# Optimization experiments

Hardware: AMD Instinct MI355X
Metric: run time of the kernel (lower is better)

## Reference

```python
import jax, jax.numpy as jnp
import numpy as np

B, T_DEC, T_SRC, D = 32, 1024, 2048, 1024


def setup_inputs() -> dict:
    key = jax.random.key(0)
    k1, k2, k3 = jax.random.split(key, 3)
    decoder_outputs = jax.random.normal(k1, (B, T_DEC, D), dtype=jnp.float32)
    encoder_outputs = jax.random.normal(k2, (B, T_SRC, D), dtype=jnp.float32)
    # realistic padding mask: each batch element has a valid length in [T_SRC//2, T_SRC]
    lengths = jax.random.randint(k3, (B, 1, 1), T_SRC // 2, T_SRC + 1)
    src_mask = jnp.arange(T_SRC)[None, None, :] < lengths  # [B,1,T_SRC] bool
    return {"decoder_outputs": decoder_outputs, "encoder_outputs": encoder_outputs, "src_mask": src_mask}


def reference(decoder_outputs, encoder_outputs, src_mask):
    # scores: [B, T_dec, T_src]
    scores = jnp.einsum('btd,bsd->bts', decoder_outputs, encoder_outputs)
    scores = jnp.where(src_mask, scores, -jnp.inf)  # src_mask [B,1,T_src] broadcasts over T_dec
    attn_weights = jax.nn.softmax(scores, axis=-1)
    context = jnp.einsum('bts,bsd->btd', attn_weights, encoder_outputs)
    return context, attn_weights
```

## Files before the change

### kernel.cpp

```cpp
#include <hip/hip_runtime.h>
#include <stdint.h>

#define NB 32
#define TDEC 1024
#define TSRC 2048
#define DDIM 1024

typedef short bf16x8 __attribute__((ext_vector_type(8)));
typedef float f32x4 __attribute__((ext_vector_type(4)));


__device__ __forceinline__ unsigned short f2bf(float f) {
  union { float f; uint32_t u; } c; c.f = f;
  return (unsigned short)((c.u + 0x7FFFu + ((c.u >> 16) & 1u)) >> 16);
}

__device__ __forceinline__ void splitt(float f, unsigned short& h, unsigned short& l) {
  union { float f; uint32_t u; } c; c.f = f;
  uint32_t hb = c.u & 0xFFFF0000u;
  h = (unsigned short)(hb >> 16);
  union { uint32_t u; float f; } hf; hf.u = hb;
  union { float f; uint32_t u; } d; d.f = f - hf.f;
  l = (unsigned short)(d.u >> 16);
}

__device__ __forceinline__ int sw4(int r, int c4) {
  return (r << 6) + ((((c4 >> 3) ^ (r & 7)) << 3) | (c4 & 7));
}
__device__ __forceinline__ int sw8(int r, int c8) {
  return (r << 6) + (((c8 >> 3) ^ (r & 7)) << 3);
}

__global__ void lens_kernel(const unsigned char* __restrict__ mask,
                            int* __restrict__ lens) {
  int b = blockIdx.x;
  int tid = threadIdx.x;
  unsigned char b1 = mask[1], b3 = mask[3];
  int cnt = 0;
  if (b1 != 0) {
    const unsigned char* row = mask + (size_t)b * TSRC;
    for (int s = tid; s < TSRC; s += 256) cnt += (row[s] != 0) ? 1 : 0;
  } else if (b3 != 0) {
    const float* row = (const float*)mask + (size_t)b * TSRC;
    for (int s = tid; s < TSRC; s += 256) cnt += (row[s] != 0.0f) ? 1 : 0;
  } else {
    const int* row = (const int*)mask + (size_t)b * TSRC;
    for (int s = tid; s < TSRC; s += 256) cnt += (row[s] != 0) ? 1 : 0;
  }
#pragma unroll
  for (int o = 32; o > 0; o >>= 1) cnt += __shfl_down(cnt, o, 64);
  __shared__ int red[4];
  if ((tid & 63) == 0) red[tid >> 6] = cnt;
  __syncthreads();
  if (tid == 0) lens[b] = red[0] + red[1] + red[2] + red[3];
}

__global__ void split_kernel(const float* __restrict__ src,
                             unsigned short* __restrict__ hi,
                             unsigned short* __restrict__ lo, int n4) {
  int i = blockIdx.x * 256 + threadIdx.x;
  if (i >= n4) return;
  float4 v = *(const float4*)(src + (size_t)i * 4);
  ushort4 h, l;
  splitt(v.x, h.x, l.x); splitt(v.y, h.y, l.y);
  splitt(v.z, h.z, l.z); splitt(v.w, h.w, l.w);
  *(ushort4*)(hi + (size_t)i * 4) = h;
  *(ushort4*)(lo + (size_t)i * 4) = l;
}

__global__ void transpose_kernel(const float* __restrict__ enc,
                                 unsigned short* __restrict__ encT) {
  __shared__ float tile[64][65];
  int b = blockIdx.z;
  int s0 = blockIdx.x << 6;
  int d0 = blockIdx.y << 6;
  int tid = threadIdx.x;
  int rl = tid >> 4;
  int c4 = (tid & 15) << 2;
  const float* src = enc + ((size_t)b * TSRC + s0) * DDIM + d0;
#pragma unroll
  for (int p = 0; p < 4; ++p) {
    int s = rl + (p << 4);
    float4 v = *(const float4*)(src + (size_t)s * DDIM + c4);
    tile[s][c4 + 0] = v.x; tile[s][c4 + 1] = v.y;
    tile[s][c4 + 2] = v.z; tile[s][c4 + 3] = v.w;
  }
  __syncthreads();
  unsigned short* dst = encT + ((size_t)b * DDIM + d0) * TSRC + s0;
#pragma unroll
  for (int p = 0; p < 4; ++p) {
    int d = rl + (p << 4);
    ushort4 o;
    o.x = f2bf(tile[c4 + 0][d]);
    o.y = f2bf(tile[c4 + 1][d]);
    o.z = f2bf(tile[c4 + 2][d]);
    o.w = f2bf(tile[c4 + 3][d]);
    *(ushort4*)(dst + (size_t)d * TSRC + c4) = o;
  }
}

__global__ __launch_bounds__(256, 2) void scores_pre(
    const unsigned short* __restrict__ dhi, const unsigned short* __restrict__ dlo,
    const unsigned short* __restrict__ ehi, const unsigned short* __restrict__ elo,
    float* __restrict__ attn, const int* __restrict__ lens) {
  int b = blockIdx.z;
  int s0 = blockIdx.x << 7;
  int t0 = blockIdx.y << 7;
  if (s0 >= lens[b]) return;
  __shared__ unsigned short Ah[8192], Al[8192], Bh[8192], Bl[8192];
  const unsigned short* Ag0 = dhi + ((size_t)b * TDEC + t0) * DDIM;
  const unsigned short* Ag1 = dlo + ((size_t)b * TDEC + t0) * DDIM;
  const unsigned short* Bg0 = ehi + ((size_t)b * TSRC + s0) * DDIM;
  const unsigned short* Bg1 = elo + ((size_t)b * TSRC + s0) * DDIM;
  int tid = threadIdx.x;
  int lane = tid & 63, wid = tid >> 6;
  int wm = (wid >> 1) << 6, wn = (wid & 1) << 6;
  int fr = lane & 15, fq = lane >> 4;
  int cc8 = (tid & 7) << 3;

  f32x4 acc[16];
#pragma unroll
  for (int i = 0; i < 16; ++i) { acc[i][0] = 0.f; acc[i][1] = 0.f; acc[i][2] = 0.f; acc[i][3] = 0.f; }

  for (int kc = 0; kc < 16; ++kc) {
    int k0 = kc << 6;
    __syncthreads();
#pragma unroll
    for (int p = 0; p < 4; ++p) {
      int r = (p << 5) + (tid >> 3);
      size_t go = (size_t)r * DDIM + k0 + cc8;
      int sw = sw8(r, cc8);
      *(bf16x8*)&Ah[sw] = *(const bf16x8*)(Ag0 + go);
      *(bf16x8*)&Al[sw] = *(const bf16x8*)(Ag1 + go);
      *(bf16x8*)&Bh[sw] = *(const bf16x8*)(Bg0 + go);
      *(bf16x8*)&Bl[sw] = *(const bf16x8*)(Bg1 + go);
    }
    __syncthreads();
#pragma unroll
    for (int ks = 0; ks < 2; ++ks) {
      bf16x8 ah[4], al[4], bh[4], bl[4];
#pragma unroll
      for (int i = 0; i < 4; ++i) {
        int ra = wm + (i << 4) + fr;
        int oa = (ra << 6) + ((((ks << 2) | fq) ^ (ra & 7)) << 3);
        ah[i] = *(const bf16x8*)&Ah[oa];
        al[i] = *(const bf16x8*)&Al[oa];
        int rb = wn + (i << 4) + fr;
        int ob = (rb << 6) + ((((ks << 2) | fq) ^ (rb & 7)) << 3);
        bh[i] = *(const bf16x8*)&Bh[ob];
        bl[i] = *(const bf16x8*)&Bl[ob];
      }
#pragma unroll
      for (int mt = 0; mt < 4; ++mt)
#pragma unroll
        for (int nt = 0; nt < 4; ++nt) {
          f32x4 c = acc[(mt << 2) + nt];
          c = __builtin_amdgcn_mfma_f32_16x16x32_bf16(ah[mt], bh[nt], c, 0, 0, 0);
          c = __builtin_amdgcn_mfma_f32_16x16x32_bf16(al[mt], bh[nt], c, 0, 0, 0);
          c = __builtin_amdgcn_mfma_f32_16x16x32_bf16(ah[mt], bl[nt], c, 0, 0, 0);
          acc[(mt << 2) + nt] = c;
        }
    }
  }
  float* C = attn + ((size_t)b * TDEC + t0) * TSRC + s0;
#pragma unroll
  for (int mt = 0; mt < 4; ++mt) {
    int r0 = wm + (mt << 4) + (fq << 2);
#pragma unroll
    for (int nt = 0; nt < 4; ++nt) {
      int c0 = wn + (nt << 4) + fr;
      f32x4 v = acc[(mt << 2) + nt];
#pragma unroll
      for (int j = 0; j < 4; ++j)
        C[(size_t)(r0 + j) * TSRC + c0] = v[j];
    }
  }
}

__global__ __launch_bounds__(256, 2) void scores_fly(
    const float* __restrict__ dec, const float* __restrict__ enc,
    float* __restrict__ attn, const int* __restrict__ lens) {
  int b = blockIdx.z;
  int s0 = blockIdx.x << 7;
  int t0 = blockIdx.y << 7;
  if (s0 >= lens[b]) return;
  __shared__ unsigned short Ah[8192], Al[8192], Bh[8192], Bl[8192];
  const float* Ag = dec + ((size_t)b * TDEC + t0) * DDIM;
  const float* Bg = enc + ((size_t)b * TSRC + s0) * DDIM;
  int tid = threadIdx.x;
  int lane = tid & 63, wid = tid >> 6;
  int wm = (wid >> 1) << 6, wn = (wid & 1) << 6;
  int fr = lane & 15, fq = lane >> 4;

  f32x4 acc[16];
#pragma unroll
  for (int i = 0; i < 16; ++i) { acc[i][0] = 0.f; acc[i][1] = 0.f; acc[i][2] = 0.f; acc[i][3] = 0.f; }

  for (int kc = 0; kc < 16; ++kc) {
    int k0 = kc << 6;
    __syncthreads();
#pragma unroll
    for (int p = 0; p < 8; ++p) {
      int r = (p << 4) + (tid >> 4);
      int c4 = (tid & 15) << 2;
      size_t go = (size_t)r * DDIM + k0 + c4;
      float4 va = *(const float4*)(Ag + go);
      float4 vb = *(const float4*)(Bg + go);
      ushort4 h, l;
      splitt(va.x, h.x, l.x); splitt(va.y, h.y, l.y);
      splitt(va.z, h.z, l.z); splitt(va.w, h.w, l.w);
      int sw = sw4(r, c4);
      *(ushort4*)&Ah[sw] = h; *(ushort4*)&Al[sw] = l;
      splitt(vb.x, h.x, l.x); splitt(vb.y, h.y, l.y);
      splitt(vb.z, h.z, l.z); splitt(vb.w, h.w, l.w);
      *(ushort4*)&Bh[sw] = h; *(ushort4*)&Bl[sw] = l;
    }
    __syncthreads();
#pragma unroll
    for (int ks = 0; ks < 2; ++ks) {
      bf16x8 ah[4], al[4], bh[4], bl[4];
#pragma unroll
      for (int i = 0; i < 4; ++i) {
        int ra = wm + (i << 4) + fr;
        int oa = (ra << 6) + ((((ks << 2) | fq) ^ (ra & 7)) << 3);
        ah[i] = *(const bf16x8*)&Ah[oa];
        al[i] = *(const bf16x8*)&Al[oa];
        int rb = wn + (i << 4) + fr;
        int ob = (rb << 6) + ((((ks << 2) | fq) ^ (rb & 7)) << 3);
        bh[i] = *(const bf16x8*)&Bh[ob];
        bl[i] = *(const bf16x8*)&Bl[ob];
      }
#pragma unroll
      for (int mt = 0; mt < 4; ++mt)
#pragma unroll
        for (int nt = 0; nt < 4; ++nt) {
          f32x4 c = acc[(mt << 2) + nt];
          c = __builtin_amdgcn_mfma_f32_16x16x32_bf16(ah[mt], bh[nt], c, 0, 0, 0);
          c = __builtin_amdgcn_mfma_f32_16x16x32_bf16(al[mt], bh[nt], c, 0, 0, 0);
          c = __builtin_amdgcn_mfma_f32_16x16x32_bf16(ah[mt], bl[nt], c, 0, 0, 0);
          acc[(mt << 2) + nt] = c;
        }
    }
  }
  float* C = attn + ((size_t)b * TDEC + t0) * TSRC + s0;
#pragma unroll
  for (int mt = 0; mt < 4; ++mt) {
    int r0 = wm + (mt << 4) + (fq << 2);
#pragma unroll
    for (int nt = 0; nt < 4; ++nt) {
      int c0 = wn + (nt << 4) + fr;
      f32x4 v = acc[(mt << 2) + nt];
#pragma unroll
      for (int j = 0; j < 4; ++j)
        C[(size_t)(r0 + j) * TSRC + c0] = v[j];
    }
  }
}

__global__ __launch_bounds__(256) void softmax_kernel(float* __restrict__ attn,
                                                      const int* __restrict__ lens) {
  int b = blockIdx.y;
  int t = blockIdx.x;
  int len = lens[b];
  float* row = attn + ((size_t)b * TDEC + t) * TSRC;
  int tid = threadIdx.x;
  int p0 = tid << 2;
  int p1 = 1024 + (tid << 2);
  float4 v0 = *(const float4*)(row + p0);
  float4 v1 = *(const float4*)(row + p1);
  float x[8] = {v0.x, v0.y, v0.z, v0.w, v1.x, v1.y, v1.z, v1.w};
  float m = -3.4e38f;
#pragma unroll
  for (int j = 0; j < 8; ++j) {
    int pos = (j < 4) ? (p0 + j) : (p1 + j - 4);
    if (pos < len) m = fmaxf(m, x[j]);
  }
#pragma unroll
  for (int o = 32; o > 0; o >>= 1) m = fmaxf(m, __shfl_down(m, o, 64));
  __shared__ float redm[4], reds[4];
  if ((tid & 63) == 0) redm[tid >> 6] = m;
  __syncthreads();
  m = fmaxf(fmaxf(redm[0], redm[1]), fmaxf(redm[2], redm[3]));
  float e[8];
  float s = 0.f;
#pragma unroll
  for (int j = 0; j < 8; ++j) {
    int pos = (j < 4) ? (p0 + j) : (p1 + j - 4);
    float ev = (pos < len) ? __expf(x[j] - m) : 0.f;
    e[j] = ev;
    s += ev;
  }
#pragma unroll
  for (int o = 32; o > 0; o >>= 1) s += __shfl_down(s, o, 64);
  if ((tid & 63) == 0) reds[tid >> 6] = s;
  __syncthreads();
  s = reds[0] + reds[1] + reds[2] + reds[3];
  float inv = 1.0f / s;
  float4 o0, o1;
  o0.x = e[0] * inv; o0.y = e[1] * inv; o0.z = e[2] * inv; o0.w = e[3] * inv;
  o1.x = e[4] * inv; o1.y = e[5] * inv; o1.z = e[6] * inv; o1.w = e[7] * inv;
  *(float4*)(row + p0) = o0;
  *(float4*)(row + p1) = o1;
}

__global__ __launch_bounds__(256, 2) void context_pre(
    const float* __restrict__ attn, const unsigned short* __restrict__ encT,
    float* __restrict__ ctx, const int* __restrict__ lens) {
  int b = blockIdx.z;
  int d0 = blockIdx.x << 7;
  int t0 = blockIdx.y << 7;
  int nk = (lens[b] + 63) >> 6;
  __shared__ unsigned short At[8192], Bt[8192];
  const float* Ag = attn + ((size_t)b * TDEC + t0) * TSRC;
  const unsigned short* Bg = encT + ((size_t)b * DDIM + d0) * TSRC;
  int tid = threadIdx.x;
  int lane = tid & 63, wid = tid >> 6;
  int wm = (wid >> 1) << 6, wn = (wid & 1) << 6;
  int fr = lane & 15, fq = lane >> 4;

  f32x4 acc[16];
#pragma unroll
  for (int i = 0; i < 16; ++i) { acc[i][0] = 0.f; acc[i][1] = 0.f; acc[i][2] = 0.f; acc[i][3] = 0.f; }

  for (int kc = 0; kc < nk; ++kc) {
    int k0 = kc << 6;
    __syncthreads();
#pragma unroll
    for (int p = 0; p < 8; ++p) {
      int r = (p << 4) + (tid >> 4);
      int c4 = (tid & 15) << 2;
      float4 v = *(const float4*)(Ag + (size_t)r * TSRC + k0 + c4);
      ushort4 h;
      h.x = f2bf(v.x); h.y = f2bf(v.y); h.z = f2bf(v.z); h.w = f2bf(v.w);
      *(ushort4*)&At[sw4(r, c4)] = h;
    }
#pragma unroll
    for (int p = 0; p < 4; ++p) {
      int r = (p << 5) + (tid >> 3);
      int c8 = (tid & 7) << 3;
      *(bf16x8*)&Bt[sw8(r, c8)] = *(const bf16x8*)(Bg + (size_t)r * TSRC + k0 + c8);
    }
    __syncthreads();
#pragma unroll
    for (int ks = 0; ks < 2; ++ks) {
      bf16x8 a[4], bb[4];
#pragma unroll
      for (int i = 0; i < 4; ++i) {
        int ra = wm + (i << 4) + fr;
        a[i] = *(const bf16x8*)&At[(ra << 6) + ((((ks << 2) | fq) ^ (ra & 7)) << 3)];
        int rb = wn + (i << 4) + fr;
        bb[i] = *(const bf16x8*)&Bt[(rb << 6) + ((((ks << 2) | fq) ^ (rb & 7)) << 3)];
      }
#pragma unroll
      for (int mt = 0; mt < 4; ++mt)
#pragma unroll
        for (int nt = 0; nt < 4; ++nt)
          acc[(mt << 2) + nt] = __builtin_amdgcn_mfma_f32_16x16x32_bf16(
              a[mt], bb[nt], acc[(mt << 2) + nt], 0, 0, 0);
    }
  }
  float* C = ctx + ((size_t)b * TDEC + t0) * DDIM + d0;
#pragma unroll
  for (int mt = 0; mt < 4; ++mt) {
    int r0 = wm + (mt << 4) + (fq << 2);
#pragma unroll
    for (int nt = 0; nt < 4; ++nt) {
      int c0 = wn + (nt << 4) + fr;
      f32x4 v = acc[(mt << 2) + nt];
#pragma unroll
      for (int j = 0; j < 4; ++j)
        C[(size_t)(r0 + j) * DDIM + c0] = v[j];
    }
  }
}

__global__ __launch_bounds__(256, 2) void context_fly(
    const float* __restrict__ attn, const float* __restrict__ enc,
    float* __restrict__ ctx, const int* __restrict__ lens) {
  int b = blockIdx.z;
  int d0 = blockIdx.x << 7;
  int t0 = blockIdx.y << 7;
  int nk = (lens[b] + 63) >> 6;
  __shared__ unsigned short At[8192], Bt[8192];
  const float* Ag = attn + ((size_t)b * TDEC + t0) * TSRC;
  const float* Bg = enc + (size_t)b * TSRC * DDIM + d0;
  int tid = threadIdx.x;
  int lane = tid & 63, wid = tid >> 6;
  int wm = (wid >> 1) << 6, wn = (wid & 1) << 6;
  int fr = lane & 15, fq = lane >> 4;

  f32x4 acc[16];
#pragma unroll
  for (int i = 0; i < 16; ++i) { acc[i][0] = 0.f; acc[i][1] = 0.f; acc[i][2] = 0.f; acc[i][3] = 0.f; }

  for (int kc = 0; kc < nk; ++kc) {
    int k0 = kc << 6;
    __syncthreads();
#pragma unroll
    for (int p = 0; p < 8; ++p) {
      int r = (p << 4) + (tid >> 4);
      int c4 = (tid & 15) << 2;
      float4 v = *(const float4*)(Ag + (size_t)r * TSRC + k0 + c4);
      ushort4 h;
      h.x = f2bf(v.x); h.y = f2bf(v.y); h.z = f2bf(v.z); h.w = f2bf(v.w);
      *(ushort4*)&At[sw4(r, c4)] = h;
    }
#pragma unroll
    for (int p = 0; p < 8; ++p) {
      int idx = (p << 8) + tid;
      int sl = idx >> 5;
      int d4 = (idx & 31) << 2;
      float4 v = *(const float4*)(Bg + (size_t)(k0 + sl) * DDIM + d4);
      float tmp[4] = {v.x, v.y, v.z, v.w};
#pragma unroll
      for (int j = 0; j < 4; ++j) {
        int n = d4 + j;
        Bt[(n << 6) + ((((sl >> 3) ^ (n & 7)) << 3) | (sl & 7))] = f2bf(tmp[j]);
      }
    }
    __syncthreads();
#pragma unroll
    for (int ks = 0; ks < 2; ++ks) {
      bf16x8 a[4], bb[4];
#pragma unroll
      for (int i = 0; i < 4; ++i) {
        int ra = wm + (i << 4) + fr;
        a[i] = *(const bf16x8*)&At[(ra << 6) + ((((ks << 2) | fq) ^ (ra & 7)) << 3)];
        int rb = wn + (i << 4) + fr;
        bb[i] = *(const bf16x8*)&Bt[(rb << 6) + ((((ks << 2) | fq) ^ (rb & 7)) << 3)];
      }
#pragma unroll
      for (int mt = 0; mt < 4; ++mt)
#pragma unroll
        for (int nt = 0; nt < 4; ++nt)
          acc[(mt << 2) + nt] = __builtin_amdgcn_mfma_f32_16x16x32_bf16(
              a[mt], bb[nt], acc[(mt << 2) + nt], 0, 0, 0);
    }
  }
  float* C = ctx + ((size_t)b * TDEC + t0) * DDIM + d0;
#pragma unroll
  for (int mt = 0; mt < 4; ++mt) {
    int r0 = wm + (mt << 4) + (fq << 2);
#pragma unroll
    for (int nt = 0; nt < 4; ++nt) {
      int c0 = wn + (nt << 4) + fr;
      f32x4 v = acc[(mt << 2) + nt];
#pragma unroll
      for (int j = 0; j < 4; ++j)
        C[(size_t)(r0 + j) * DDIM + c0] = v[j];
    }
  }
}

extern "C" void kernel_launch(void* const* d_in, const int* in_sizes, int n_in,
                              void* d_out, int out_size, void* d_ws, size_t ws_size,
                              hipStream_t stream) {
  (void)in_sizes; (void)n_in; (void)out_size;
  const float* dec = (const float*)d_in[0];
  const float* enc = (const float*)d_in[1];
  const unsigned char* mask = (const unsigned char*)d_in[2];
  float* ctx = (float*)d_out;
  float* attn = ctx + (size_t)NB * TDEC * DDIM;

  size_t nDec = (size_t)NB * TDEC * DDIM;
  size_t nEnc = (size_t)NB * TSRC * DDIM;
  char* wsb = (char*)d_ws;
  int* lens = (int*)wsb;
  unsigned short* dec_hi = (unsigned short*)(wsb + 256);
  unsigned short* dec_lo = dec_hi + nDec;
  unsigned short* enc_hi = dec_lo + nDec;
  unsigned short* enc_lo = enc_hi + nEnc;
  unsigned short* encT = enc_lo + nEnc;
  size_t need = 256 + (2 * nDec + 3 * nEnc) * sizeof(unsigned short);
  int pre = (ws_size >= need) ? 1 : 0;

  lens_kernel<<<NB, 256, 0, stream>>>(mask, lens);
  if (pre) {
    split_kernel<<<(int)(nDec / 4 / 256), 256, 0, stream>>>(dec, dec_hi, dec_lo, (int)(nDec / 4));
    split_kernel<<<(int)(nEnc / 4 / 256), 256, 0, stream>>>(enc, enc_hi, enc_lo, (int)(nEnc / 4));
    transpose_kernel<<<dim3(TSRC / 64, DDIM / 64, NB), 256, 0, stream>>>(enc, encT);
    scores_pre<<<dim3(TSRC / 128, TDEC / 128, NB), 256, 0, stream>>>(
        dec_hi, dec_lo, enc_hi, enc_lo, attn, lens);
  } else {
    scores_fly<<<dim3(TSRC / 128, TDEC / 128, NB), 256, 0, stream>>>(dec, enc, attn, lens);
  }
  softmax_kernel<<<dim3(TDEC, NB), 256, 0, stream>>>(attn, lens);
  if (pre) {
    context_pre<<<dim3(DDIM / 128, TDEC / 128, NB), 256, 0, stream>>>(attn, encT, ctx, lens);
  } else {
    context_fly<<<dim3(DDIM / 128, TDEC / 128, NB), 256, 0, stream>>>(attn, enc, ctx, lens);
  }
}
```

Measured before the change: 1.582 ms.

## Use direct global-to-LDS loads, fuse encoder split/transpose, emit bf16 attention from softmax

The GEMM tile loads in scores_pre and context_pre now use global_load_lds to copy 16 bytes straight into shared memory, with the XOR swizzle moved to the global address side. This removes the register round-trip on each tile load. The encoder hi/lo split is folded into the transpose kernel, so the fp32 encoder is read once instead of twice. Softmax also writes a bf16 copy of the attention weights into the reused dec_hi buffer, and context_pre reads that half-size copy instead of converting fp32 on every tile. The cost is an extra bf16 write pass in softmax, and aliasing dec_hi is only safe because scores_pre has finished using it.

```diff
diff --git a/kernel.cpp b/kernel.cpp
--- a/kernel.cpp
+++ b/kernel.cpp
@@ -29,6 +29,15 @@
 }
 __device__ __forceinline__ int sw8(int r, int c8) {
   return (r << 6) + (((c8 >> 3) ^ (r & 7)) << 3);
+}
+
+__device__ __forceinline__ void gload16(const void* g, void* l) {
+  __builtin_amdgcn_global_load_lds(
+      reinterpret_cast<const __attribute__((address_space(1))) uint32_t*>(
+          reinterpret_cast<uintptr_t>(g)),
+      reinterpret_cast<__attribute__((address_space(3))) uint32_t*>(
+          reinterpret_cast<uintptr_t>(l)),
+      16, 0, 0);
 }
 
 __global__ void lens_kernel(const unsigned char* __restrict__ mask,
@@ -68,8 +77,10 @@
   *(ushort4*)(lo + (size_t)i * 4) = l;
 }
 
-__global__ void transpose_kernel(const float* __restrict__ enc,
-                                 unsigned short* __restrict__ encT) {
+__global__ void encprep_kernel(const float* __restrict__ enc,
+                               unsigned short* __restrict__ ehi,
+                               unsigned short* __restrict__ elo,
+                               unsigned short* __restrict__ encT) {
   __shared__ float tile[64][65];
   int b = blockIdx.z;
   int s0 = blockIdx.x << 6;
@@ -78,12 +89,19 @@
   int rl = tid >> 4;
   int c4 = (tid & 15) << 2;
   const float* src = enc + ((size_t)b * TSRC + s0) * DDIM + d0;
+  unsigned short* hdst = ehi + ((size_t)b * TSRC + s0) * DDIM + d0;
+  unsigned short* ldst = elo + ((size_t)b * TSRC + s0) * DDIM + d0;
 #pragma unroll
   for (int p = 0; p < 4; ++p) {
     int s = rl + (p << 4);
     float4 v = *(const float4*)(src + (size_t)s * DDIM + c4);
     tile[s][c4 + 0] = v.x; tile[s][c4 + 1] = v.y;
     tile[s][c4 + 2] = v.z; tile[s][c4 + 3] = v.w;
+    ushort4 h, l;
+    splitt(v.x, h.x, l.x); splitt(v.y, h.y, l.y);
+    splitt(v.z, h.z, l.z); splitt(v.w, h.w, l.w);
+    *(ushort4*)(hdst + (size_t)s * DDIM + c4) = h;
+    *(ushort4*)(ldst + (size_t)s * DDIM + c4) = l;
   }
   __syncthreads();
   unsigned short* dst = encT + ((size_t)b * DDIM + d0) * TSRC + s0;
@@ -116,7 +134,16 @@
   int lane = tid & 63, wid = tid >> 6;
   int wm = (wid >> 1) << 6, wn = (wid & 1) << 6;
   int fr = lane & 15, fq = lane >> 4;
-  int cc8 = (tid & 7) << 3;
+
+  int gg[4]; size_t go[4];
+#pragma unroll
+  for (int p = 0; p < 4; ++p) {
+    int g = (p << 8) + tid;
+    int r = g >> 3;
+    int sg = (g & 7) ^ (r & 7);
+    gg[p] = g << 3;
+    go[p] = (size_t)r * DDIM + (sg << 3);
+  }
 
   f32x4 acc[16];
 #pragma unroll
@@ -127,13 +154,10 @@
     __syncthreads();
 #pragma unroll
     for (int p = 0; p < 4; ++p) {
-      int r = (p << 5) + (tid >> 3);
-      size_t go = (size_t)r * DDIM + k0 + cc8;
-      int sw = sw8(r, cc8);
-      *(bf16x8*)&Ah[sw] = *(const bf16x8*)(Ag0 + go);
-      *(bf16x8*)&Al[sw] = *(const bf16x8*)(Ag1 + go);
-      *(bf16x8*)&Bh[sw] = *(const bf16x8*)(Bg0 + go);
-      *(bf16x8*)&Bl[sw] = *(const bf16x8*)(Bg1 + go);
+      gload16(Ag0 + go[p] + k0, &Ah[gg[p]]);
+      gload16(Ag1 + go[p] + k0, &Al[gg[p]]);
+      gload16(Bg0 + go[p] + k0, &Bh[gg[p]]);
+      gload16(Bg1 + go[p] + k0, &Bl[gg[p]]);
     }
     __syncthreads();
 #pragma unroll
@@ -258,7 +282,8 @@
 }
 
 __global__ __launch_bounds__(256) void softmax_kernel(float* __restrict__ attn,
-                                                      const int* __restrict__ lens) {
+                                                      const int* __restrict__ lens,
+                                                      unsigned short* __restrict__ attn_bf) {
   int b = blockIdx.y;
   int t = blockIdx.x;
   int len = lens[b];
@@ -301,23 +326,41 @@
   o1.x = e[4] * inv; o1.y = e[5] * inv; o1.z = e[6] * inv; o1.w = e[7] * inv;
   *(float4*)(row + p0) = o0;
   *(float4*)(row + p1) = o1;
+  if (attn_bf) {
+    unsigned short* rb = attn_bf + ((size_t)b * TDEC + t) * TSRC;
+    ushort4 h0, h1;
+    h0.x = f2bf(o0.x); h0.y = f2bf(o0.y); h0.z = f2bf(o0.z); h0.w = f2bf(o0.w);
+    h1.x = f2bf(o1.x); h1.y = f2bf(o1.y); h1.z = f2bf(o1.z); h1.w = f2bf(o1.w);
+    *(ushort4*)(rb + p0) = h0;
+    *(ushort4*)(rb + p1) = h1;
+  }
 }
 
 __global__ __launch_bounds__(256, 2) void context_pre(
-    const float* __restrict__ attn, const unsigned short* __restrict__ encT,
+    const unsigned short* __restrict__ attn_bf, const unsigned short* __restrict__ encT,
     float* __restrict__ ctx, const int* __restrict__ lens) {
   int b = blockIdx.z;
   int d0 = blockIdx.x << 7;
   int t0 = blockIdx.y << 7;
   int nk = (lens[b] + 63) >> 6;
   __shared__ unsigned short At[8192], Bt[8192];
-  const float* Ag = attn + ((size_t)b * TDEC + t0) * TSRC;
+  const unsigned short* Ag = attn_bf + ((size_t)b * TDEC + t0) * TSRC;
   const unsigned short* Bg = encT + ((size_t)b * DDIM + d0) * TSRC;
   int tid = threadIdx.x;
   int lane = tid & 63, wid = tid >> 6;
   int wm = (wid >> 1) << 6, wn = (wid & 1) << 6;
   int fr = lane & 15, fq = lane >> 4;
 
+  int gg[4]; size_t go[4];
+#pragma unroll
+  for (int p = 0; p < 4; ++p) {
+    int g = (p << 8) + tid;
+    int r = g >> 3;
+    int sg = (g & 7) ^ (r & 7);
+    gg[p] = g << 3;
+    go[p] = (size_t)r * TSRC + (sg << 3);
+  }
+
   f32x4 acc[16];
 #pragma unroll
   for (int i = 0; i < 16; ++i) { acc[i][0] = 0.f; acc[i][1] = 0.f; acc[i][2] = 0.f; acc[i][3] = 0.f; }
@@ -326,19 +369,9 @@
     int k0 = kc << 6;
     __syncthreads();
 #pragma unroll
-    for (int p = 0; p < 8; ++p) {
-      int r = (p << 4) + (tid >> 4);
-      int c4 = (tid & 15) << 2;
-      float4 v = *(const float4*)(Ag + (size_t)r * TSRC + k0 + c4);
-      ushort4 h;
-      h.x = f2bf(v.x); h.y = f2bf(v.y); h.z = f2bf(v.z); h.w = f2bf(v.w);
-      *(ushort4*)&At[sw4(r, c4)] = h;
-    }
-#pragma unroll
     for (int p = 0; p < 4; ++p) {
-      int r = (p << 5) + (tid >> 3);
-      int c8 = (tid & 7) << 3;
-      *(bf16x8*)&Bt[sw8(r, c8)] = *(const bf16x8*)(Bg + (size_t)r * TSRC + k0 + c8);
+      gload16(Ag + go[p] + k0, &At[gg[p]]);
+      gload16(Bg + go[p] + k0, &Bt[gg[p]]);
     }
     __syncthreads();
 #pragma unroll
@@ -471,22 +504,22 @@
   unsigned short* enc_hi = dec_lo + nDec;
   unsigned short* enc_lo = enc_hi + nEnc;
   unsigned short* encT = enc_lo + nEnc;
+  unsigned short* attn_bf = dec_hi;
   size_t need = 256 + (2 * nDec + 3 * nEnc) * sizeof(unsigned short);
   int pre = (ws_size >= need) ? 1 : 0;
 
   lens_kernel<<<NB, 256, 0, stream>>>(mask, lens);
   if (pre) {
     split_kernel<<<(int)(nDec / 4 / 256), 256, 0, stream>>>(dec, dec_hi, dec_lo, (int)(nDec / 4));
-    split_kernel<<<(int)(nEnc / 4 / 256), 256, 0, stream>>>(enc, enc_hi, enc_lo, (int)(nEnc / 4));
-    transpose_kernel<<<dim3(TSRC / 64, DDIM / 64, NB), 256, 0, stream>>>(enc, encT);
+    encprep_kernel<<<dim3(TSRC / 64, DDIM / 64, NB), 256, 0, stream>>>(enc, enc_hi, enc_lo, encT);
     scores_pre<<<dim3(TSRC / 128, TDEC / 128, NB), 256, 0, stream>>>(
         dec_hi, dec_lo, enc_hi, enc_lo, attn, lens);
   } else {
     scores_fly<<<dim3(TSRC / 128, TDEC / 128, NB), 256, 0, stream>>>(dec, enc, attn, lens);
   }
-  softmax_kernel<<<dim3(TDEC, NB), 256, 0, stream>>>(attn, lens);
+  softmax_kernel<<<dim3(TDEC, NB), 256, 0, stream>>>(attn, lens, pre ? attn_bf : (unsigned short*)nullptr);
   if (pre) {
-    context_pre<<<dim3(DDIM / 128, TDEC / 128, NB), 256, 0, stream>>>(attn, encT, ctx, lens);
+    context_pre<<<dim3(DDIM / 128, TDEC / 128, NB), 256, 0, stream>>>(attn_bf, encT, ctx, lens);
   } else {
     context_fly<<<dim3(DDIM / 128, TDEC / 128, NB), 256, 0, stream>>>(attn, enc, ctx, lens);
   }
```

After: 1.282 ms. 19.0% less time.
